# Kernel optimization log

Measured on AMD Instinct MI355X. Metric: run time of the kernel, lower is better.

Reference implementation:

```python
import jax, jax.numpy as jnp
import numpy as np

B, R, D = 16, 2048, 512
H2, NREL = 2 * D, 2048  # relation_mlp hidden = 2*d_model, output = n_relations
MIN_PROB = 0.1          # early-stop probability threshold from the torch code


def setup_inputs() -> dict:
    key = jax.random.key(0)
    ks = jax.random.split(key, 8)
    sc = lambda k, shp: jax.random.normal(k, shp, jnp.float32) * 0.02
    return {
        "rel_encoding": jax.random.normal(ks[0], (B, R, D), jnp.float32),
        "na_emb": jax.random.normal(ks[1], (D,), jnp.float32),
        "v_w": sc(ks[2], (D, D)), "v_b": jnp.zeros((D,), jnp.float32),
        "o_w": sc(ks[3], (D, D)), "o_b": jnp.zeros((D,), jnp.float32),
        "ln_g": jnp.ones((D,), jnp.float32), "ln_b": jnp.zeros((D,), jnp.float32),
        "w1": sc(ks[4], (H2, D)), "b1": jnp.zeros((H2,), jnp.float32),
        "w2": sc(ks[5], (NREL, H2)), "b2": jnp.zeros((NREL,), jnp.float32),
    }


def _ln(x, g, b, eps=1e-5):
    m = jnp.mean(x, axis=-1, keepdims=True)
    v = jnp.var(x, axis=-1, keepdims=True)
    return (x - m) * jax.lax.rsqrt(v + eps) * g + b


def reference(rel_encoding, na_emb, v_w, v_b, o_w, o_b, ln_g, ln_b, w1, b1, w2, b2):
    # Cross-attention with a single key/value token: softmax over a length-1 axis
    # is identically 1, so attn_out = out_proj(v_proj(kv)) for every query position.
    x = rel_encoding                                         # [B,R,D]
    attn = (x @ v_w.T + v_b) @ o_w.T + o_b                   # [B,R,D]

    def step_logits(state):                                  # state broadcasts to [B,R,D]
        h = _ln(attn + state, ln_g, ln_b)                    # residual + layernorm
        return jax.nn.relu(h @ w1.T + b1) @ w2.T + b2        # [B,R,NREL]

    # step 0: query is the na_embedding
    p0 = jax.nn.softmax(step_logits(na_emb), axis=-1)
    m0 = jnp.max(p0, axis=-1)
    i0 = jnp.argmax(p0, axis=-1)
    cont0 = (i0 != 0) & (m0 >= MIN_PROB)                     # else break before step 0 emits

    # step 1: last appended state is the relation encoding itself
    p1 = jax.nn.softmax(step_logits(x), axis=-1)
    m1 = jnp.max(p1, axis=-1)
    i1 = jnp.argmax(p1, axis=-1)
    cont1 = cont0 & (i1 != 0) & (m1 >= MIN_PROB)

    # rule_score = prod of accepted step probs; 0.0 if no step accepted
    scores = jnp.where(cont0, jnp.where(cont1, m0 * m1, m0), 0.0)  # [B,R]
    lengths = cont0.astype(jnp.int32) + cont1.astype(jnp.int32)    # ragged rule lengths
    return scores, i0, i1, lengths
```

## Files before the change

kernel.cpp:

```cpp
#include <hip/hip_runtime.h>
#include <math.h>

#define MTOT 32768
#define DD   512
#define HHD  1024
#define NRELN 2048
#define SCA  64.f
#define SCB  1024.f
#define INVS (1.f / 65536.f)

typedef _Float16 h8 __attribute__((ext_vector_type(8)));
typedef float    f4 __attribute__((ext_vector_type(4)));

__device__ inline void fsplit(float x, _Float16& h, _Float16& l) {
  _Float16 t = (_Float16)x;
  h = t;
  l = (_Float16)(x - (float)t);
}

__device__ inline void omerge(float& M, float& S, int& I, float m2, float s2, int i2) {
  if (m2 > M || (m2 == M && i2 < I)) { S = S * __expf(M - m2) + s2; M = m2; I = i2; }
  else                               { S += s2 * __expf(m2 - M); }
}


__global__ void prep_wvo_split(const float* __restrict__ vw, const float* __restrict__ ow,
                               _Float16* __restrict__ wh, _Float16* __restrict__ wl) {
  int idx = blockIdx.x * 256 + threadIdx.x;
  int k = idx & 511;
  int n = idx >> 9;
  float s = 0.f;
  for (int j = 0; j < DD; ++j) s += ow[n * DD + j] * vw[j * DD + k];
  fsplit(s * SCB, wh[n * DD + k], wl[n * DD + k]);
}

__global__ void prep_cvec(const float* __restrict__ ow, const float* __restrict__ vb,
                          const float* __restrict__ ob, float* __restrict__ c) {
  int i = blockIdx.x * 256 + threadIdx.x;
  if (i < DD) {
    float s = ob[i];
    for (int k = 0; k < DD; ++k) s += ow[i * DD + k] * vb[k];
    c[i] = s;
  }
}

__global__ void prep_w1p_split(const float* __restrict__ w1, const float* __restrict__ g,
                               _Float16* __restrict__ wh, _Float16* __restrict__ wl) {
  int idx = blockIdx.x * 256 + threadIdx.x;
  int k = idx & 511;
  int n = idx >> 9;
  fsplit(w1[n * DD + k] * g[k] * SCB, wh[n * DD + k], wl[n * DD + k]);
}

__global__ void prep_b1p(const float* __restrict__ w1, const float* __restrict__ lnb,
                         const float* __restrict__ b1, float* __restrict__ b1p) {
  int n = blockIdx.x * 256 + threadIdx.x;
  if (n < HHD) {
    float s = b1[n];
    for (int k = 0; k < DD; ++k) s += w1[n * DD + k] * lnb[k];
    b1p[n] = s;
  }
}

__global__ void prep_w2_split(const float* __restrict__ w2,
                              _Float16* __restrict__ wh, _Float16* __restrict__ wl) {
  int idx = blockIdx.x * 256 + threadIdx.x;
  int k = idx & 1023;
  int n = idx >> 10;
  fsplit(w2[n * HHD + k] * SCB, wh[n * HHD + k], wl[n * HHD + k]);
}

__global__ void split_x(const float* __restrict__ src, _Float16* __restrict__ h,
                        _Float16* __restrict__ l) {
  int idx = (blockIdx.x * 256 + threadIdx.x) * 8;
  float4 a = *(const float4*)(src + idx);
  float4 b = *(const float4*)(src + idx + 4);
  float vv[8] = {a.x, a.y, a.z, a.w, b.x, b.y, b.z, b.w};
  _Float16 hh[8], ll[8];
#pragma unroll
  for (int i = 0; i < 8; ++i) fsplit(vv[i] * SCA, hh[i], ll[i]);
  *(h8*)(h + idx) = *(h8*)hh;
  *(h8*)(l + idx) = *(h8*)ll;
}

template <int MODE, int KDIM, int NTOT>
__global__ __launch_bounds__(256) void gemm_split(
    const _Float16* __restrict__ Ah, const _Float16* __restrict__ Al,
    const _Float16* __restrict__ Bh, const _Float16* __restrict__ Bl,
    const float* __restrict__ bias,
    float* __restrict__ outF,
    _Float16* __restrict__ outHh, _Float16* __restrict__ outHl,
    float* __restrict__ pM, float* __restrict__ pS, float* __restrict__ pI,
    int row0) {
  __shared__ __align__(16) _Float16 sA[2][128][40];
  __shared__ __align__(16) _Float16 sB[2][128][40];
  const int t = threadIdx.x;
  const int lane = t & 63;
  const int wv = t >> 6;
  const int wr = wv & 1, wc = wv >> 1;
  const int q = lane >> 4, l16 = lane & 15;
  const int m0 = blockIdx.x << 7;
  const int n0 = blockIdx.y << 7;
  f4 acc[4][4];
#pragma unroll
  for (int i = 0; i < 4; ++i)
#pragma unroll
    for (int j = 0; j < 4; ++j) {
      acc[i][j].x = 0.f; acc[i][j].y = 0.f; acc[i][j].z = 0.f; acc[i][j].w = 0.f;
    }
  for (int k0 = 0; k0 < KDIM; k0 += 32) {
    __syncthreads();
#pragma unroll
    for (int it = 0; it < 8; ++it) {
      const int arr = it >> 1;
      const int row = ((it & 1) << 6) | (t >> 2);
      const int kc = (t & 3) << 3;
      const _Float16* sp = (arr == 0) ? Ah : (arr == 1) ? Al : (arr == 2) ? Bh : Bl;
      const int base = (arr < 2) ? m0 : n0;
      h8 v = *(const h8*)(sp + (size_t)(base + row) * KDIM + (k0 + kc));
      _Float16* dp = (arr == 0) ? &sA[0][0][0] : (arr == 1) ? &sA[1][0][0]
                   : (arr == 2) ? &sB[0][0][0] : &sB[1][0][0];
      *(h8*)(dp + row * 40 + kc) = v;
    }
    __syncthreads();
    h8 afh[4], afl[4];
#pragma unroll
    for (int i = 0; i < 4; ++i) {
      const int ar = (wr << 6) + (i << 4) + l16;
      afh[i] = *(const h8*)&sA[0][ar][q << 3];
      afl[i] = *(const h8*)&sA[1][ar][q << 3];
    }
#pragma unroll
    for (int j = 0; j < 4; ++j) {
      const int br = (wc << 6) + (j << 4) + l16;
      h8 bh = *(const h8*)&sB[0][br][q << 3];
      h8 bl = *(const h8*)&sB[1][br][q << 3];
#pragma unroll
      for (int i = 0; i < 4; ++i) {
        acc[i][j] = __builtin_amdgcn_mfma_f32_16x16x32_f16(afh[i], bh, acc[i][j], 0, 0, 0);
        acc[i][j] = __builtin_amdgcn_mfma_f32_16x16x32_f16(afh[i], bl, acc[i][j], 0, 0, 0);
        acc[i][j] = __builtin_amdgcn_mfma_f32_16x16x32_f16(afl[i], bh, acc[i][j], 0, 0, 0);
      }
    }
  }
  int gcol[4];
  float bb[4];
#pragma unroll
  for (int j = 0; j < 4; ++j) {
    gcol[j] = n0 + (wc << 6) + (j << 4) + l16;
    bb[j] = bias[gcol[j]];
  }
  if constexpr (MODE == 0) {
#pragma unroll
    for (int i = 0; i < 4; ++i)
#pragma unroll
      for (int rr = 0; rr < 4; ++rr) {
        const int rowt = (wr << 6) + (i << 4) + (q << 2) + rr;
#pragma unroll
        for (int j = 0; j < 4; ++j)
          outF[(size_t)(m0 + rowt) * NTOT + gcol[j]] = acc[i][j][rr] * INVS + bb[j];
      }
  } else if constexpr (MODE == 1) {
#pragma unroll
    for (int i = 0; i < 4; ++i)
#pragma unroll
      for (int rr = 0; rr < 4; ++rr) {
        const int rowt = (wr << 6) + (i << 4) + (q << 2) + rr;
#pragma unroll
        for (int j = 0; j < 4; ++j) {
          float v = fmaxf(acc[i][j][rr] * INVS + bb[j], 0.f) * SCA;
          _Float16 hh, ll;
          fsplit(v, hh, ll);
          outHh[(size_t)(m0 + rowt) * NTOT + gcol[j]] = hh;
          outHl[(size_t)(m0 + rowt) * NTOT + gcol[j]] = ll;
        }
      }
  } else {
    const int slot = blockIdx.y * 2 + wc;
#pragma unroll
    for (int i = 0; i < 4; ++i)
#pragma unroll
      for (int rr = 0; rr < 4; ++rr) {
        float v0 = acc[i][0][rr] * INVS + bb[0];
        float M = v0, S = 1.f;
        int I = gcol[0];
#pragma unroll
        for (int j = 1; j < 4; ++j) {
          float v = acc[i][j][rr] * INVS + bb[j];
          omerge(M, S, I, v, 1.f, gcol[j]);
        }
#pragma unroll
        for (int m = 1; m <= 8; m <<= 1) {
          float M2 = __shfl_xor(M, m);
          float S2 = __shfl_xor(S, m);
          int   I2 = __shfl_xor(I, m);
          omerge(M, S, I, M2, S2, I2);
        }
        if (l16 == 0) {
          const int grow = row0 + m0 + (wr << 6) + (i << 4) + (q << 2) + rr;
          pM[(size_t)slot * MTOT + grow] = M;
          pS[(size_t)slot * MTOT + grow] = S;
          pI[(size_t)slot * MTOT + grow] = (float)I;
        }
      }
  }
}

__global__ __launch_bounds__(256) void ln_split(
    const float* __restrict__ A, const float* __restrict__ X,
    const float* __restrict__ na, _Float16* __restrict__ yh,
    _Float16* __restrict__ yl, int row0, int step) {
  int t = threadIdx.x;
  int lane = t & 63;
  int w = t >> 6;
  int r = blockIdx.x * 4 + w;
  const float* ap = A + (size_t)r * DD + lane * 8;
  const float* sp = step ? (X + (size_t)(row0 + r) * DD + lane * 8) : (na + lane * 8);
  float v[8];
  float s = 0.f, qq = 0.f;
#pragma unroll
  for (int i = 0; i < 8; ++i) {
    v[i] = ap[i] + sp[i];
    s += v[i];
    qq += v[i] * v[i];
  }
#pragma unroll
  for (int m = 1; m <= 32; m <<= 1) {
    s  += __shfl_xor(s, m);
    qq += __shfl_xor(qq, m);
  }
  float mu = s * (1.f / DD);
  float var = qq * (1.f / DD) - mu * mu;
  float rsd = 1.f / sqrtf(var + 1e-5f);
  _Float16 hh[8], ll[8];
#pragma unroll
  for (int i = 0; i < 8; ++i) fsplit((v[i] - mu) * rsd * SCA, hh[i], ll[i]);
  *(h8*)(yh + (size_t)r * DD + lane * 8) = *(h8*)hh;
  *(h8*)(yl + (size_t)r * DD + lane * 8) = *(h8*)ll;
}

__global__ void finalize_k(const float* __restrict__ pM0, const float* __restrict__ pS0,
                           const float* __restrict__ pI0, const float* __restrict__ pM1,
                           const float* __restrict__ pS1, const float* __restrict__ pI1,
                           float* __restrict__ out) {
  int r = blockIdx.x * 256 + threadIdx.x;
  float M = pM0[r], S = pS0[r];
  int I = (int)pI0[r];
  for (int s = 1; s < 32; ++s) {
    size_t o = (size_t)s * MTOT + r;
    omerge(M, S, I, pM0[o], pS0[o], (int)pI0[o]);
  }
  float m0v = 1.f / S;
  int i0v = I;
  M = pM1[r]; S = pS1[r]; I = (int)pI1[r];
  for (int s = 1; s < 32; ++s) {
    size_t o = (size_t)s * MTOT + r;
    omerge(M, S, I, pM1[o], pS1[o], (int)pI1[o]);
  }
  float m1v = 1.f / S;
  int i1v = I;
  bool c0 = (i0v != 0) && (m0v >= 0.1f);
  bool c1 = c0 && (i1v != 0) && (m1v >= 0.1f);
  out[r] = c0 ? (c1 ? m0v * m1v : m0v) : 0.f;
  out[MTOT + r] = (float)i0v;
  out[2 * MTOT + r] = (float)i1v;
  out[3 * MTOT + r] = (float)((c0 ? 1 : 0) + (c1 ? 1 : 0));
}

extern "C" void kernel_launch(void* const* d_in, const int* in_sizes, int n_in,
                              void* d_out, int out_size, void* d_ws, size_t ws_size,
                              hipStream_t stream) {
  const float* X   = (const float*)d_in[0];
  const float* na  = (const float*)d_in[1];
  const float* vw  = (const float*)d_in[2];
  const float* vb  = (const float*)d_in[3];
  const float* ow  = (const float*)d_in[4];
  const float* ob  = (const float*)d_in[5];
  const float* lng = (const float*)d_in[6];
  const float* lnb = (const float*)d_in[7];
  const float* w1  = (const float*)d_in[8];
  const float* b1  = (const float*)d_in[9];
  const float* w2  = (const float*)d_in[10];
  const float* b2  = (const float*)d_in[11];
  float* out = (float*)d_out;

  char* p = (char*)d_ws;
  auto alloc = [&](size_t bytes) -> void* {
    void* r = (void*)p;
    p += (bytes + 255) & ~(size_t)255;
    return r;
  };
  _Float16* wvo_h = (_Float16*)alloc(512 * 512 * 2);
  _Float16* wvo_l = (_Float16*)alloc(512 * 512 * 2);
  float*    cvec  = (float*)alloc(512 * 4);
  _Float16* w1p_h = (_Float16*)alloc(1024 * 512 * 2);
  _Float16* w1p_l = (_Float16*)alloc(1024 * 512 * 2);
  float*    b1p   = (float*)alloc(1024 * 4);
  _Float16* w2_h  = (_Float16*)alloc(2048 * 1024 * 2);
  _Float16* w2_l  = (_Float16*)alloc(2048 * 1024 * 2);
  float* pM0 = (float*)alloc((size_t)32 * MTOT * 4);
  float* pS0 = (float*)alloc((size_t)32 * MTOT * 4);
  float* pI0 = (float*)alloc((size_t)32 * MTOT * 4);
  float* pM1 = (float*)alloc((size_t)32 * MTOT * 4);
  float* pS1 = (float*)alloc((size_t)32 * MTOT * 4);
  float* pI1 = (float*)alloc((size_t)32 * MTOT * 4);
  size_t fixed = (size_t)(p - (char*)d_ws);
  size_t remain = ws_size > fixed + 8192 ? ws_size - fixed - 8192 : 0;
  int chunk = (int)(remain / 10240);
  chunk &= ~127;
  if (chunk < 128) chunk = 128;
  if (chunk > MTOT) chunk = MTOT;
  _Float16* xs_h = (_Float16*)alloc((size_t)chunk * 512 * 2);
  _Float16* xs_l = (_Float16*)alloc((size_t)chunk * 512 * 2);
  float*    Abuf = (float*)alloc((size_t)chunk * 512 * 4);
  _Float16* y_h  = (_Float16*)alloc((size_t)chunk * 512 * 2);
  _Float16* y_l  = (_Float16*)alloc((size_t)chunk * 512 * 2);
  _Float16* H_h  = (_Float16*)alloc((size_t)chunk * 1024 * 2);
  _Float16* H_l  = (_Float16*)alloc((size_t)chunk * 1024 * 2);

  prep_wvo_split<<<1024, 256, 0, stream>>>(vw, ow, wvo_h, wvo_l);
  prep_cvec<<<2, 256, 0, stream>>>(ow, vb, ob, cvec);
  prep_w1p_split<<<2048, 256, 0, stream>>>(w1, lng, w1p_h, w1p_l);
  prep_b1p<<<4, 256, 0, stream>>>(w1, lnb, b1, b1p);
  prep_w2_split<<<8192, 256, 0, stream>>>(w2, w2_h, w2_l);

  for (int row0 = 0; row0 < MTOT; row0 += chunk) {
    int rows = (MTOT - row0 < chunk) ? (MTOT - row0) : chunk;
    split_x<<<rows / 4, 256, 0, stream>>>(X + (size_t)row0 * 512, xs_h, xs_l);
    gemm_split<0, 512, 512><<<dim3(rows / 128, 4), 256, 0, stream>>>(
        xs_h, xs_l, wvo_h, wvo_l, cvec, Abuf, nullptr, nullptr,
        nullptr, nullptr, nullptr, 0);
    for (int s = 0; s < 2; ++s) {
      ln_split<<<rows / 4, 256, 0, stream>>>(Abuf, X, na, y_h, y_l, row0, s);
      gemm_split<1, 512, 1024><<<dim3(rows / 128, 8), 256, 0, stream>>>(
          y_h, y_l, w1p_h, w1p_l, b1p, nullptr, H_h, H_l,
          nullptr, nullptr, nullptr, 0);
      gemm_split<2, 1024, 2048><<<dim3(rows / 128, 16), 256, 0, stream>>>(
          H_h, H_l, w2_h, w2_l, b2, nullptr, nullptr, nullptr,
          s == 0 ? pM0 : pM1, s == 0 ? pS0 : pS1, s == 0 ? pI0 : pI1, row0);
    }
  }
  finalize_k<<<MTOT / 256, 256, 0, stream>>>(pM0, pS0, pI0, pM1, pS1, pI1, out);
}
```

Measured before the change: 1.700 ms.

## Use 32x32 MFMA with direct global-to-LDS loads and fuse dual layernorm

The split-fp16 GEMM switches from 16x16x32 to 32x32x16 MFMA tiles. Operand tiles now go straight from global memory into an XOR-swizzled LDS layout through global_load_lds, replacing register-staged copies into padded rows. The softmax partial reduction computes the max first and then a single sum, and the two per-step layernorm launches are merged into one kernel that writes both normalized inputs, reusing the xs buffers. The aim is to raise MFMA throughput and cut LDS and launch overhead, at the cost of more complex indexing and a risk of swizzle or layout mistakes.

```diff
diff --git a/kernel.cpp b/kernel.cpp
--- a/kernel.cpp
+++ b/kernel.cpp
@@ -9,18 +9,24 @@
 #define SCB  1024.f
 #define INVS (1.f / 65536.f)
 
-typedef _Float16 h8 __attribute__((ext_vector_type(8)));
-typedef float    f4 __attribute__((ext_vector_type(4)));
-
-__device__ inline void fsplit(float x, _Float16& h, _Float16& l) {
+typedef _Float16 h8  __attribute__((ext_vector_type(8)));
+typedef float    f16v __attribute__((ext_vector_type(16)));
+
+__device__ __forceinline__ void fsplit(float x, _Float16& h, _Float16& l) {
   _Float16 t = (_Float16)x;
   h = t;
   l = (_Float16)(x - (float)t);
 }
 
-__device__ inline void omerge(float& M, float& S, int& I, float m2, float s2, int i2) {
+__device__ __forceinline__ void omerge(float& M, float& S, int& I, float m2, float s2, int i2) {
   if (m2 > M || (m2 == M && i2 < I)) { S = S * __expf(M - m2) + s2; M = m2; I = i2; }
   else                               { S += s2 * __expf(m2 - M); }
+}
+
+__device__ __forceinline__ void gld16(const _Float16* g, _Float16* l) {
+  __builtin_amdgcn_global_load_lds(
+      (const __attribute__((address_space(1))) void*)g,
+      (__attribute__((address_space(3))) void*)l, 16, 0, 0);
 }
 
 
@@ -92,112 +98,115 @@
     _Float16* __restrict__ outHh, _Float16* __restrict__ outHl,
     float* __restrict__ pM, float* __restrict__ pS, float* __restrict__ pI,
     int row0) {
-  __shared__ __align__(16) _Float16 sA[2][128][40];
-  __shared__ __align__(16) _Float16 sB[2][128][40];
+  __shared__ __align__(16) _Float16 sA[2][128][32];
+  __shared__ __align__(16) _Float16 sB[2][128][32];
   const int t = threadIdx.x;
   const int lane = t & 63;
   const int wv = t >> 6;
   const int wr = wv & 1, wc = wv >> 1;
-  const int q = lane >> 4, l16 = lane & 15;
+  const int l31 = lane & 31, half = lane >> 5;
   const int m0 = blockIdx.x << 7;
   const int n0 = blockIdx.y << 7;
-  f4 acc[4][4];
-#pragma unroll
-  for (int i = 0; i < 4; ++i)
-#pragma unroll
-    for (int j = 0; j < 4; ++j) {
-      acc[i][j].x = 0.f; acc[i][j].y = 0.f; acc[i][j].z = 0.f; acc[i][j].w = 0.f;
-    }
+
+  const _Float16* gsp = (wv == 0) ? Ah : (wv == 1) ? Al : (wv == 2) ? Bh : Bl;
+  const int gb = (wv < 2) ? m0 : n0;
+  _Float16* lbase = (wv == 0) ? &sA[0][0][0] : (wv == 1) ? &sA[1][0][0]
+                  : (wv == 2) ? &sB[0][0][0] : &sB[1][0][0];
+  const int srow = lane >> 2;
+  const int schunk = (lane & 3) ^ ((lane >> 3) & 3);
+  const _Float16* gptr0 = gsp + (size_t)(gb + srow) * KDIM + schunk * 8;
+
+  f16v acc[2][2] = {};
+  const int swz = (lane >> 1) & 3;
+
   for (int k0 = 0; k0 < KDIM; k0 += 32) {
     __syncthreads();
 #pragma unroll
-    for (int it = 0; it < 8; ++it) {
-      const int arr = it >> 1;
-      const int row = ((it & 1) << 6) | (t >> 2);
-      const int kc = (t & 3) << 3;
-      const _Float16* sp = (arr == 0) ? Ah : (arr == 1) ? Al : (arr == 2) ? Bh : Bl;
-      const int base = (arr < 2) ? m0 : n0;
-      h8 v = *(const h8*)(sp + (size_t)(base + row) * KDIM + (k0 + kc));
-      _Float16* dp = (arr == 0) ? &sA[0][0][0] : (arr == 1) ? &sA[1][0][0]
-                   : (arr == 2) ? &sB[0][0][0] : &sB[1][0][0];
-      *(h8*)(dp + row * 40 + kc) = v;
+    for (int it = 0; it < 8; ++it)
+      gld16(gptr0 + k0 + (size_t)(it * 16) * KDIM, lbase + it * 512);
+    __syncthreads();
+#pragma unroll
+    for (int ks = 0; ks < 2; ++ks) {
+      const int pos = (((ks << 1) + half) ^ swz) << 3;
+      h8 af_h[2], af_l[2], bf_h[2], bf_l[2];
+#pragma unroll
+      for (int i = 0; i < 2; ++i) {
+        const int mr = wr * 64 + i * 32 + l31;
+        af_h[i] = *(const h8*)&sA[0][mr][pos];
+        af_l[i] = *(const h8*)&sA[1][mr][pos];
+      }
+#pragma unroll
+      for (int j = 0; j < 2; ++j) {
+        const int nr = wc * 64 + j * 32 + l31;
+        bf_h[j] = *(const h8*)&sB[0][nr][pos];
+        bf_l[j] = *(const h8*)&sB[1][nr][pos];
+      }
+#pragma unroll
+      for (int j = 0; j < 2; ++j)
+#pragma unroll
+        for (int i = 0; i < 2; ++i) {
+          acc[i][j] = __builtin_amdgcn_mfma_f32_32x32x16_f16(af_h[i], bf_h[j], acc[i][j], 0, 0, 0);
+          acc[i][j] = __builtin_amdgcn_mfma_f32_32x32x16_f16(af_h[i], bf_l[j], acc[i][j], 0, 0, 0);
+          acc[i][j] = __builtin_amdgcn_mfma_f32_32x32x16_f16(af_l[i], bf_h[j], acc[i][j], 0, 0, 0);
+        }
     }
-    __syncthreads();
-    h8 afh[4], afl[4];
-#pragma unroll
-    for (int i = 0; i < 4; ++i) {
-      const int ar = (wr << 6) + (i << 4) + l16;
-      afh[i] = *(const h8*)&sA[0][ar][q << 3];
-      afl[i] = *(const h8*)&sA[1][ar][q << 3];
-    }
-#pragma unroll
-    for (int j = 0; j < 4; ++j) {
-      const int br = (wc << 6) + (j << 4) + l16;
-      h8 bh = *(const h8*)&sB[0][br][q << 3];
-      h8 bl = *(const h8*)&sB[1][br][q << 3];
-#pragma unroll
-      for (int i = 0; i < 4; ++i) {
-        acc[i][j] = __builtin_amdgcn_mfma_f32_16x16x32_f16(afh[i], bh, acc[i][j], 0, 0, 0);
-        acc[i][j] = __builtin_amdgcn_mfma_f32_16x16x32_f16(afh[i], bl, acc[i][j], 0, 0, 0);
-        acc[i][j] = __builtin_amdgcn_mfma_f32_16x16x32_f16(afl[i], bh, acc[i][j], 0, 0, 0);
-      }
-    }
-  }
-  int gcol[4];
-  float bb[4];
-#pragma unroll
-  for (int j = 0; j < 4; ++j) {
-    gcol[j] = n0 + (wc << 6) + (j << 4) + l16;
-    bb[j] = bias[gcol[j]];
+  }
+
+  float bb[2];
+  int gc[2];
+#pragma unroll
+  for (int j = 0; j < 2; ++j) {
+    gc[j] = n0 + wc * 64 + j * 32 + l31;
+    bb[j] = bias[gc[j]];
   }
   if constexpr (MODE == 0) {
 #pragma unroll
-    for (int i = 0; i < 4; ++i)
-#pragma unroll
-      for (int rr = 0; rr < 4; ++rr) {
-        const int rowt = (wr << 6) + (i << 4) + (q << 2) + rr;
-#pragma unroll
-        for (int j = 0; j < 4; ++j)
-          outF[(size_t)(m0 + rowt) * NTOT + gcol[j]] = acc[i][j][rr] * INVS + bb[j];
+    for (int i = 0; i < 2; ++i)
+#pragma unroll
+      for (int r = 0; r < 16; ++r) {
+        const int row = m0 + wr * 64 + i * 32 + (r & 3) + 8 * (r >> 2) + 4 * half;
+#pragma unroll
+        for (int j = 0; j < 2; ++j)
+          outF[(size_t)row * NTOT + gc[j]] = acc[i][j][r] * INVS + bb[j];
       }
   } else if constexpr (MODE == 1) {
 #pragma unroll
-    for (int i = 0; i < 4; ++i)
-#pragma unroll
-      for (int rr = 0; rr < 4; ++rr) {
-        const int rowt = (wr << 6) + (i << 4) + (q << 2) + rr;
-#pragma unroll
-        for (int j = 0; j < 4; ++j) {
-          float v = fmaxf(acc[i][j][rr] * INVS + bb[j], 0.f) * SCA;
+    for (int i = 0; i < 2; ++i)
+#pragma unroll
+      for (int r = 0; r < 16; ++r) {
+        const int row = m0 + wr * 64 + i * 32 + (r & 3) + 8 * (r >> 2) + 4 * half;
+#pragma unroll
+        for (int j = 0; j < 2; ++j) {
+          float v = fmaxf(acc[i][j][r] * INVS + bb[j], 0.f) * SCA;
           _Float16 hh, ll;
           fsplit(v, hh, ll);
-          outHh[(size_t)(m0 + rowt) * NTOT + gcol[j]] = hh;
-          outHl[(size_t)(m0 + rowt) * NTOT + gcol[j]] = ll;
+          outHh[(size_t)row * NTOT + gc[j]] = hh;
+          outHl[(size_t)row * NTOT + gc[j]] = ll;
         }
       }
   } else {
     const int slot = blockIdx.y * 2 + wc;
 #pragma unroll
-    for (int i = 0; i < 4; ++i)
-#pragma unroll
-      for (int rr = 0; rr < 4; ++rr) {
-        float v0 = acc[i][0][rr] * INVS + bb[0];
-        float M = v0, S = 1.f;
-        int I = gcol[0];
-#pragma unroll
-        for (int j = 1; j < 4; ++j) {
-          float v = acc[i][j][rr] * INVS + bb[j];
-          omerge(M, S, I, v, 1.f, gcol[j]);
+    for (int i = 0; i < 2; ++i)
+#pragma unroll
+      for (int r = 0; r < 16; ++r) {
+        float v0 = acc[i][0][r] * INVS + bb[0];
+        float v1 = acc[i][1][r] * INVS + bb[1];
+        float M;
+        int I;
+        if (v0 >= v1) { M = v0; I = gc[0]; }
+        else          { M = v1; I = gc[1]; }
+#pragma unroll
+        for (int sh = 1; sh <= 16; sh <<= 1) {
+          float M2 = __shfl_xor(M, sh);
+          int   I2 = __shfl_xor(I, sh);
+          if (M2 > M || (M2 == M && I2 < I)) { M = M2; I = I2; }
         }
-#pragma unroll
-        for (int m = 1; m <= 8; m <<= 1) {
-          float M2 = __shfl_xor(M, m);
-          float S2 = __shfl_xor(S, m);
-          int   I2 = __shfl_xor(I, m);
-          omerge(M, S, I, M2, S2, I2);
-        }
-        if (l16 == 0) {
-          const int grow = row0 + m0 + (wr << 6) + (i << 4) + (q << 2) + rr;
+        float S = __expf(v0 - M) + __expf(v1 - M);
+#pragma unroll
+        for (int sh = 1; sh <= 16; sh <<= 1) S += __shfl_xor(S, sh);
+        if (l31 == 0) {
+          const int grow = row0 + m0 + wr * 64 + i * 32 + (r & 3) + 8 * (r >> 2) + 4 * half;
           pM[(size_t)slot * MTOT + grow] = M;
           pS[(size_t)slot * MTOT + grow] = S;
           pI[(size_t)slot * MTOT + grow] = (float)I;
@@ -206,37 +215,46 @@
   }
 }
 
-__global__ __launch_bounds__(256) void ln_split(
+__global__ __launch_bounds__(256) void ln_dual(
     const float* __restrict__ A, const float* __restrict__ X,
-    const float* __restrict__ na, _Float16* __restrict__ yh,
-    _Float16* __restrict__ yl, int row0, int step) {
+    const float* __restrict__ na,
+    _Float16* __restrict__ y0h, _Float16* __restrict__ y0l,
+    _Float16* __restrict__ y1h, _Float16* __restrict__ y1l, int row0) {
   int t = threadIdx.x;
   int lane = t & 63;
   int w = t >> 6;
   int r = blockIdx.x * 4 + w;
   const float* ap = A + (size_t)r * DD + lane * 8;
-  const float* sp = step ? (X + (size_t)(row0 + r) * DD + lane * 8) : (na + lane * 8);
-  float v[8];
-  float s = 0.f, qq = 0.f;
+  const float* xp = X + (size_t)(row0 + r) * DD + lane * 8;
+  const float* np = na + lane * 8;
+  float v0[8], v1[8];
+  float s0 = 0.f, q0 = 0.f, s1 = 0.f, q1 = 0.f;
 #pragma unroll
   for (int i = 0; i < 8; ++i) {
-    v[i] = ap[i] + sp[i];
-    s += v[i];
-    qq += v[i] * v[i];
+    float a = ap[i];
+    v0[i] = a + np[i];
+    v1[i] = a + xp[i];
+    s0 += v0[i]; q0 += v0[i] * v0[i];
+    s1 += v1[i]; q1 += v1[i] * v1[i];
   }
 #pragma unroll
   for (int m = 1; m <= 32; m <<= 1) {
-    s  += __shfl_xor(s, m);
-    qq += __shfl_xor(qq, m);
-  }
-  float mu = s * (1.f / DD);
-  float var = qq * (1.f / DD) - mu * mu;
-  float rsd = 1.f / sqrtf(var + 1e-5f);
-  _Float16 hh[8], ll[8];
-#pragma unroll
-  for (int i = 0; i < 8; ++i) fsplit((v[i] - mu) * rsd * SCA, hh[i], ll[i]);
-  *(h8*)(yh + (size_t)r * DD + lane * 8) = *(h8*)hh;
-  *(h8*)(yl + (size_t)r * DD + lane * 8) = *(h8*)ll;
+    s0 += __shfl_xor(s0, m); q0 += __shfl_xor(q0, m);
+    s1 += __shfl_xor(s1, m); q1 += __shfl_xor(q1, m);
+  }
+  float mu0 = s0 * (1.f / DD), mu1 = s1 * (1.f / DD);
+  float rs0 = 1.f / sqrtf(q0 * (1.f / DD) - mu0 * mu0 + 1e-5f);
+  float rs1 = 1.f / sqrtf(q1 * (1.f / DD) - mu1 * mu1 + 1e-5f);
+  _Float16 h0[8], l0[8], h1[8], l1[8];
+#pragma unroll
+  for (int i = 0; i < 8; ++i) {
+    fsplit((v0[i] - mu0) * rs0 * SCA, h0[i], l0[i]);
+    fsplit((v1[i] - mu1) * rs1 * SCA, h1[i], l1[i]);
+  }
+  *(h8*)(y0h + (size_t)r * DD + lane * 8) = *(h8*)h0;
+  *(h8*)(y0l + (size_t)r * DD + lane * 8) = *(h8*)l0;
+  *(h8*)(y1h + (size_t)r * DD + lane * 8) = *(h8*)h1;
+  *(h8*)(y1l + (size_t)r * DD + lane * 8) = *(h8*)l1;
 }
 
 __global__ void finalize_k(const float* __restrict__ pM0, const float* __restrict__ pS0,
@@ -313,10 +331,12 @@
   _Float16* xs_h = (_Float16*)alloc((size_t)chunk * 512 * 2);
   _Float16* xs_l = (_Float16*)alloc((size_t)chunk * 512 * 2);
   float*    Abuf = (float*)alloc((size_t)chunk * 512 * 4);
-  _Float16* y_h  = (_Float16*)alloc((size_t)chunk * 512 * 2);
-  _Float16* y_l  = (_Float16*)alloc((size_t)chunk * 512 * 2);
+  _Float16* y0_h = (_Float16*)alloc((size_t)chunk * 512 * 2);
+  _Float16* y0_l = (_Float16*)alloc((size_t)chunk * 512 * 2);
   _Float16* H_h  = (_Float16*)alloc((size_t)chunk * 1024 * 2);
   _Float16* H_l  = (_Float16*)alloc((size_t)chunk * 1024 * 2);
+  _Float16* y1_h = xs_h;
+  _Float16* y1_l = xs_l;
 
   prep_wvo_split<<<1024, 256, 0, stream>>>(vw, ow, wvo_h, wvo_l);
   prep_cvec<<<2, 256, 0, stream>>>(ow, vb, ob, cvec);
@@ -330,11 +350,11 @@
     gemm_split<0, 512, 512><<<dim3(rows / 128, 4), 256, 0, stream>>>(
         xs_h, xs_l, wvo_h, wvo_l, cvec, Abuf, nullptr, nullptr,
         nullptr, nullptr, nullptr, 0);
+    ln_dual<<<rows / 4, 256, 0, stream>>>(Abuf, X, na, y0_h, y0_l, y1_h, y1_l, row0);
     for (int s = 0; s < 2; ++s) {
-      ln_split<<<rows / 4, 256, 0, stream>>>(Abuf, X, na, y_h, y_l, row0, s);
       gemm_split<1, 512, 1024><<<dim3(rows / 128, 8), 256, 0, stream>>>(
-          y_h, y_l, w1p_h, w1p_l, b1p, nullptr, H_h, H_l,
-          nullptr, nullptr, nullptr, 0);
+          s == 0 ? y0_h : y1_h, s == 0 ? y0_l : y1_l, w1p_h, w1p_l, b1p,
+          nullptr, H_h, H_l, nullptr, nullptr, nullptr, 0);
       gemm_split<2, 1024, 2048><<<dim3(rows / 128, 16), 256, 0, stream>>>(
           H_h, H_l, w2_h, w2_l, b2, nullptr, nullptr, nullptr,
           s == 0 ? pM0 : pM1, s == 0 ? pS0 : pS1, s == 0 ? pI0 : pI1, row0);
```

Result: no change. 1.680 ms (-1.2%).
